# Kernel tuning notes

Measured on AMD Instinct MI355X. Metric: run time of the kernel, lower is better.

## Reference

```python
import jax, jax.numpy as jnp
import numpy as np

B, C_IN, H, W = 8, 64, 64, 64
C_OUT = 128
K, STRIDE, PAD = 3, 1, 1
GRID_MIN, GRID_MAX, NUM_GRIDS = -2.0, 2.0, 8
FEAT = C_IN * K * K  # 576


def setup_inputs() -> dict:
    key = jax.random.key(0)
    k1, k2, k3 = jax.random.split(key, 3)
    x = jax.random.normal(k1, (B, C_IN, H, W), dtype=jnp.float32)
    grid = jnp.linspace(GRID_MIN, GRID_MAX, NUM_GRIDS, dtype=jnp.float32)
    spline_weight = jax.random.normal(k2, (FEAT * NUM_GRIDS, C_OUT), dtype=jnp.float32) * 0.1
    # nn.Linear default init ~ U(-1/sqrt(in), 1/sqrt(in)); stored as (in, out) for x @ W
    bound = 1.0 / np.sqrt(FEAT)
    kw, kb = jax.random.split(k3)
    base_w = jax.random.uniform(kw, (FEAT, C_OUT), dtype=jnp.float32, minval=-bound, maxval=bound)
    base_b = jax.random.uniform(kb, (C_OUT,), dtype=jnp.float32, minval=-bound, maxval=bound)
    return {"x": x, "grid": grid, "spline_weight": spline_weight,
            "base_w": base_w, "base_b": base_b}


def reference(x, grid, spline_weight, base_w, base_b):
    b, c, h, w = x.shape
    # F.unfold equivalent: patches in (channel, kh, kw) channel-major order.
    patches = jax.lax.conv_general_dilated_patches(
        x, filter_shape=(K, K), window_strides=(STRIDE, STRIDE),
        padding=((PAD, PAD), (PAD, PAD)))  # [B, C*K*K, H', W']
    oh, ow = patches.shape[2], patches.shape[3]
    # -> [B*L, FEAT] rows, matching unfold().transpose(1,2).reshape(...)
    p = patches.reshape(b, FEAT, oh * ow).transpose(0, 2, 1).reshape(-1, FEAT)
    # RBF basis expansion: exp(-((x - g) / h)^2), h = grid spacing
    denom = (GRID_MAX - GRID_MIN) / (NUM_GRIDS - 1)
    basis = jnp.exp(-(((p[:, :, None] - grid) / denom) ** 2))  # [N, FEAT, G]
    ret = basis.reshape(p.shape[0], FEAT * NUM_GRIDS) @ spline_weight  # [N, C_OUT]
    ret = ret + jax.nn.silu(p) @ base_w + base_b
    # [B, L, C_OUT] -> [B, C_OUT, H', W']
    out = ret.reshape(b, oh * ow, C_OUT).transpose(0, 2, 1).reshape(b, C_OUT, oh, ow)
    return out
```

## Files before the change

kernel.cpp:

```cpp
#include <hip/hip_runtime.h>

#define C_IN   64
#define HW_DIM 64
#define C_OUT  128
#define NG     8
#define KSPL   4608
#define BM     64
#define NSPL_STEPS 72
#define NSTEPS 81
#define NPAD   66
#define NEXP   (8 * C_IN * NPAD * NPAD)

#define WT_BYTES 1327104
#define XE_OFF   WT_BYTES
#define XE_BYTES (NEXP * NG * 2)
#define SE_OFF   (XE_OFF + XE_BYTES)

typedef __attribute__((ext_vector_type(8))) __bf16 bf16x8;
typedef __attribute__((ext_vector_type(4))) float  f32x4;

__global__ __launch_bounds__(256)
void prep_wt(const float* __restrict__ sw, const float* __restrict__ bw,
             __bf16* __restrict__ wt3)
{
  const int step = blockIdx.x;
  const int t    = threadIdx.x;
  const int wc   = t >> 6;
  const int lane = t & 63;
  const int l15  = lane & 15;
  const int g4   = lane >> 4;
#pragma unroll
  for (int n = 0; n < 2; ++n)
#pragma unroll
    for (int ks = 0; ks < 2; ++ks) {
      const int co = wc * 32 + n * 16 + l15;
      bf16x8 v;
#pragma unroll
      for (int e = 0; e < 8; ++e) {
        const int k = step * 64 + ks * 32 + g4 * 8 + e;
        float f;
        if (k < KSPL) f = sw[(size_t)k * C_OUT + co];
        else          f = bw[(size_t)(k - KSPL) * C_OUT + co];
        v[e] = (__bf16)f;
      }
      *(bf16x8*)(wt3 + (size_t)step * 8192 + wc * 2048 + (n * 2 + ks) * 512
                 + lane * 8) = v;
    }
}

__global__ __launch_bounds__(256)
void expand(const float* __restrict__ x, const float* __restrict__ grid,
            __bf16* __restrict__ xe, __bf16* __restrict__ se)
{
  const int idx = blockIdx.x * 256 + threadIdx.x;
  if (idx >= NEXP) return;
  const int xp = idx % NPAD;
  const int r  = idx / NPAD;
  const int yp = r % NPAD;
  const int bc = r / NPAD;

  float p = 0.f;
  if (xp >= 1 && xp <= HW_DIM && yp >= 1 && yp <= HW_DIM)
    p = x[(size_t)bc * (HW_DIM * HW_DIM) + (yp - 1) * HW_DIM + (xp - 1)];

  bf16x8 v;
#pragma unroll
  for (int g = 0; g < NG; ++g) {
    const float z = 1.75f * (p - grid[g]);
    v[g] = (__bf16)__expf(-z * z);
  }
  *(bf16x8*)(xe + (size_t)idx * NG) = v;
  const float e = __expf(-p);
  se[idx] = (__bf16)(p * __builtin_amdgcn_rcpf(1.f + e));
}

static __device__ __forceinline__ void gload16(const __bf16* g, __bf16* l) {
  __builtin_amdgcn_global_load_lds(
      (const __attribute__((address_space(1))) void*)g,
      (__attribute__((address_space(3))) void*)l, 16, 0, 0);
}

#define WAITBAR6() do {                                      \
    asm volatile("s_waitcnt vmcnt(6)" ::: "memory");         \
    __builtin_amdgcn_s_barrier();                            \
    __builtin_amdgcn_sched_barrier(0);                       \
  } while (0)

__global__ __launch_bounds__(256, 2)
void kan_gemm(const __bf16* __restrict__ xe, const __bf16* __restrict__ se,
              const __bf16* __restrict__ wt3, const float* __restrict__ base_b,
              float* __restrict__ out)
{
  __shared__ __align__(16) __bf16 As[3][BM][64];
  __shared__ int tbl[576];

  const int t    = threadIdx.x;
  const int lane = t & 63;
  const int wid  = t >> 6;
  const int l15  = lane & 15;
  const int g4   = lane >> 4;

  const int bid = blockIdx.x;
  const int swz = (bid & 7) * 64 + (bid >> 3);
  const int b   = swz >> 6;
  const int y0  = swz & 63;

  for (int f = t; f < 576; f += 256) {
    const int c  = f / 9;
    const int j  = f - 9 * c;
    const int kh = j / 3;
    const int kw = j - 3 * kh;
    tbl[f] = c * 4356 + kh * 66 + kw;
  }

  const int ROW = b * 278784 + y0 * 66;

  const int qsrc  = (lane & 7) ^ ((lane >> 3) & 7);
  const int pbase = (wid << 3) + (lane >> 3);

  f32x4 acc[2][4];
#pragma unroll
  for (int n = 0; n < 2; ++n)
#pragma unroll
    for (int m = 0; m < 4; ++m)
      acc[n][m] = f32x4{0.f, 0.f, 0.f, 0.f};

  auto stageA = [&](int buf, int step) {
    const int off = ROW + tbl[step * 8 + qsrc] + pbase;
    __bf16* dst = &As[buf][0][0] + t * 8;
    gload16(xe + (size_t)off * 8,        dst);
    gload16(xe + (size_t)(off + 32) * 8, dst + 2048);
  };

  auto loadB = [&](bf16x8 (&wf)[2][2], int step) {
    const __bf16* wb = wt3 + (size_t)step * 8192 + wid * 2048 + lane * 8;
#pragma unroll
    for (int n = 0; n < 2; ++n)
#pragma unroll
      for (int ks = 0; ks < 2; ++ks)
        wf[n][ks] = *(const bf16x8*)(wb + (n * 2 + ks) * 512);
  };

  auto compute = [&](int buf, bf16x8 (&wf)[2][2]) {
    bf16x8 xf[4][2];
#pragma unroll
    for (int ks = 0; ks < 2; ++ks)
#pragma unroll
      for (int m = 0; m < 4; ++m) {
        const int pr = m * 16 + l15;
        xf[m][ks] = *(const bf16x8*)(&As[buf][pr][(((ks * 4 + g4) ^ (pr & 7)) * 8)]);
      }
#pragma unroll
    for (int ks = 0; ks < 2; ++ks)
#pragma unroll
      for (int n = 0; n < 2; ++n)
#pragma unroll
        for (int m = 0; m < 4; ++m)
          acc[n][m] = __builtin_amdgcn_mfma_f32_16x16x32_bf16(
              wf[n][ks], xf[m][ks], acc[n][m], 0, 0, 0);
  };

  __syncthreads();

  bf16x8 wA[2][2], wB[2][2], wC[2][2];
  stageA(0, 0); loadB(wA, 0);
  stageA(1, 1); loadB(wB, 1);
  WAITBAR6();

  for (int s = 0; s < 69; s += 3) {
    stageA(2, s + 2); loadB(wC, s + 2);
    compute(0, wA);
    WAITBAR6();
    stageA(0, s + 3); loadB(wA, s + 3);
    compute(1, wB);
    WAITBAR6();
    stageA(1, s + 4); loadB(wB, s + 4);
    compute(2, wC);
    WAITBAR6();
  }
  stageA(2, 71); loadB(wC, 71);
  compute(0, wA);
  WAITBAR6();
  compute(1, wB);
  asm volatile("s_waitcnt vmcnt(0)" ::: "memory");
  __builtin_amdgcn_s_barrier();
  __builtin_amdgcn_sched_barrier(0);
  compute(2, wC);

  const int ROWs = ROW + (t & 63);
  auto stageBase = [&](int buf, int bs) {
    const int px = t & 63;
#pragma unroll
    for (int h = 0; h < 2; ++h) {
      const int q = (t >> 6) + h * 4;
      bf16x8 v;
#pragma unroll
      for (int jj = 0; jj < 8; ++jj) {
        const int f = (bs - NSPL_STEPS) * 64 + q * 8 + jj;
        v[jj] = se[(size_t)(ROWs + tbl[f])];
      }
      *(bf16x8*)(&As[buf][px][(q ^ (px & 7)) * 8]) = v;
    }
  };

  stageBase(0, NSPL_STEPS);
  __syncthreads();
  for (int bs = NSPL_STEPS; bs < NSTEPS; ++bs) {
    const int cb = (bs - NSPL_STEPS) & 1;
    if (bs + 1 < NSTEPS) stageBase(cb ^ 1, bs + 1);
    loadB(wA, bs);
    compute(cb, wA);
    __syncthreads();
  }

#pragma unroll
  for (int n = 0; n < 2; ++n) {
    const int co = wid * 32 + n * 16 + g4 * 4;
#pragma unroll
    for (int m = 0; m < 4; ++m) {
      const int pl = m * 16 + l15;
      float* o = out + (size_t)(b * C_OUT + co) * 4096 + y0 * 64 + pl;
#pragma unroll
      for (int i = 0; i < 4; ++i)
        o[(size_t)i * 4096] = acc[n][m][i] + base_b[co + i];
    }
  }
}

extern "C" void kernel_launch(void* const* d_in, const int* in_sizes, int n_in,
                              void* d_out, int out_size, void* d_ws, size_t ws_size,
                              hipStream_t stream) {
  const float* x    = (const float*)d_in[0];
  const float* grid = (const float*)d_in[1];
  const float* sw   = (const float*)d_in[2];
  const float* bw   = (const float*)d_in[3];
  const float* bb   = (const float*)d_in[4];
  float* out = (float*)d_out;

  __bf16* wt3 = (__bf16*)d_ws;
  __bf16* xe  = (__bf16*)((char*)d_ws + XE_OFF);
  __bf16* se  = (__bf16*)((char*)d_ws + SE_OFF);

  prep_wt<<<NSTEPS, 256, 0, stream>>>(sw, bw, wt3);
  expand<<<(NEXP + 255) / 256, 256, 0, stream>>>(x, grid, xe, se);
  kan_gemm<<<512, 256, 0, stream>>>(xe, se, wt3, bb, out);
}
```

Before: 78.85 us.

## Double GEMM block tile to two output rows with 512 threads

Each block now covers two output rows (128 pixels) with 8 waves instead of one row with 4 waves. Each pair of waves shares the same weight columns, and the grid halves to 256 blocks. The goal is more reuse of the staged tiles and fewer blocks re-reading weights. In exchange the shared tile doubles in size, and with only 256 blocks occupancy or load balance across CUs may suffer.

```diff
diff --git a/kernel.cpp b/kernel.cpp
--- a/kernel.cpp
+++ b/kernel.cpp
@@ -5,7 +5,7 @@
 #define C_OUT  128
 #define NG     8
 #define KSPL   4608
-#define BM     64
+#define BM     128
 #define NSPL_STEPS 72
 #define NSTEPS 81
 #define NPAD   66
@@ -25,7 +25,7 @@
 {
   const int step = blockIdx.x;
   const int t    = threadIdx.x;
-  const int wc   = t >> 6;
+  const int nq   = t >> 6;
   const int lane = t & 63;
   const int l15  = lane & 15;
   const int g4   = lane >> 4;
@@ -33,7 +33,7 @@
   for (int n = 0; n < 2; ++n)
 #pragma unroll
     for (int ks = 0; ks < 2; ++ks) {
-      const int co = wc * 32 + n * 16 + l15;
+      const int co = nq * 32 + n * 16 + l15;
       bf16x8 v;
 #pragma unroll
       for (int e = 0; e < 8; ++e) {
@@ -43,7 +43,7 @@
         else          f = bw[(size_t)(k - KSPL) * C_OUT + co];
         v[e] = (__bf16)f;
       }
-      *(bf16x8*)(wt3 + (size_t)step * 8192 + wc * 2048 + (n * 2 + ks) * 512
+      *(bf16x8*)(wt3 + (size_t)step * 8192 + nq * 2048 + (n * 2 + ks) * 512
                  + lane * 8) = v;
     }
 }
@@ -86,7 +86,7 @@
     __builtin_amdgcn_sched_barrier(0);                       \
   } while (0)
 
-__global__ __launch_bounds__(256, 2)
+__global__ __launch_bounds__(512, 2)
 void kan_gemm(const __bf16* __restrict__ xe, const __bf16* __restrict__ se,
               const __bf16* __restrict__ wt3, const float* __restrict__ base_b,
               float* __restrict__ out)
@@ -99,13 +99,15 @@
   const int wid  = t >> 6;
   const int l15  = lane & 15;
   const int g4   = lane >> 4;
+  const int mh   = wid >> 2;
+  const int nq   = wid & 3;
 
   const int bid = blockIdx.x;
-  const int swz = (bid & 7) * 64 + (bid >> 3);
-  const int b   = swz >> 6;
-  const int y0  = swz & 63;
-
-  for (int f = t; f < 576; f += 256) {
+  const int swz = (bid & 7) * 32 + (bid >> 3);
+  const int b   = swz >> 5;
+  const int y0  = (swz & 31) * 2;
+
+  for (int f = t; f < 576; f += 512) {
     const int c  = f / 9;
     const int j  = f - 9 * c;
     const int kh = j / 3;
@@ -115,8 +117,8 @@
 
   const int ROW = b * 278784 + y0 * 66;
 
-  const int qsrc  = (lane & 7) ^ ((lane >> 3) & 7);
-  const int pbase = (wid << 3) + (lane >> 3);
+  const int qsrc = (t & 7) ^ ((t >> 3) & 7);
+  const int xcol = t >> 3;
 
   f32x4 acc[2][4];
 #pragma unroll
@@ -126,14 +128,14 @@
       acc[n][m] = f32x4{0.f, 0.f, 0.f, 0.f};
 
   auto stageA = [&](int buf, int step) {
-    const int off = ROW + tbl[step * 8 + qsrc] + pbase;
+    const int off = ROW + tbl[step * 8 + qsrc] + xcol;
     __bf16* dst = &As[buf][0][0] + t * 8;
     gload16(xe + (size_t)off * 8,        dst);
-    gload16(xe + (size_t)(off + 32) * 8, dst + 2048);
+    gload16(xe + (size_t)(off + 66) * 8, dst + 4096);
   };
 
   auto loadB = [&](bf16x8 (&wf)[2][2], int step) {
-    const __bf16* wb = wt3 + (size_t)step * 8192 + wid * 2048 + lane * 8;
+    const __bf16* wb = wt3 + (size_t)step * 8192 + nq * 2048 + lane * 8;
 #pragma unroll
     for (int n = 0; n < 2; ++n)
 #pragma unroll
@@ -147,7 +149,7 @@
     for (int ks = 0; ks < 2; ++ks)
 #pragma unroll
       for (int m = 0; m < 4; ++m) {
-        const int pr = m * 16 + l15;
+        const int pr = mh * 64 + m * 16 + l15;
         xf[m][ks] = *(const bf16x8*)(&As[buf][pr][(((ks * 4 + g4) ^ (pr & 7)) * 8)]);
       }
 #pragma unroll
@@ -187,19 +189,18 @@
   __builtin_amdgcn_sched_barrier(0);
   compute(2, wC);
 
-  const int ROWs = ROW + (t & 63);
   auto stageBase = [&](int buf, int bs) {
-    const int px = t & 63;
 #pragma unroll
     for (int h = 0; h < 2; ++h) {
-      const int q = (t >> 6) + h * 4;
+      const int px    = h * 64 + (t >> 3);
+      const int gslot = t & 7;
       bf16x8 v;
 #pragma unroll
       for (int jj = 0; jj < 8; ++jj) {
-        const int f = (bs - NSPL_STEPS) * 64 + q * 8 + jj;
-        v[jj] = se[(size_t)(ROWs + tbl[f])];
+        const int f = (bs - NSPL_STEPS) * 64 + qsrc * 8 + jj;
+        v[jj] = se[(size_t)(ROW + tbl[f] + (px >> 6) * 66 + (px & 63))];
       }
-      *(bf16x8*)(&As[buf][px][(q ^ (px & 7)) * 8]) = v;
+      *(bf16x8*)(&As[buf][px][gslot * 8]) = v;
     }
   };
 
@@ -215,11 +216,12 @@
 
 #pragma unroll
   for (int n = 0; n < 2; ++n) {
-    const int co = wid * 32 + n * 16 + g4 * 4;
+    const int co = nq * 32 + n * 16 + g4 * 4;
 #pragma unroll
     for (int m = 0; m < 4; ++m) {
-      const int pl = m * 16 + l15;
-      float* o = out + (size_t)(b * C_OUT + co) * 4096 + y0 * 64 + pl;
+      const int y = y0 + mh;
+      const int xcoord = m * 16 + l15;
+      float* o = out + (size_t)(b * C_OUT + co) * 4096 + y * 64 + xcoord;
 #pragma unroll
       for (int i = 0; i < 4; ++i)
         o[(size_t)i * 4096] = acc[n][m][i] + base_b[co + i];
@@ -243,5 +245,5 @@
 
   prep_wt<<<NSTEPS, 256, 0, stream>>>(sw, bw, wt3);
   expand<<<(NEXP + 255) / 256, 256, 0, stream>>>(x, grid, xe, se);
-  kan_gemm<<<512, 256, 0, stream>>>(xe, se, wt3, bb, out);
-}
+  kan_gemm<<<256, 512, 0, stream>>>(xe, se, wt3, bb, out);
+}
```

Result: slower. 97.55 us (+23.7%).

## Double spline K-step width to 128 and split base weights into separate layout

Applied to the files above, without the earlier changes.

The spline GEMM main loop now processes 128 K-elements per pipeline stage (36 stages instead of 72). The weight prep is reorganised into a 128-wide spline layout plus a separate 64-wide base section, and a new XOR swizzle is applied to the wider LDS tile. MFMA sections are wrapped in s_setprio to favour matrix issue. The goal is to halve the barrier and wait count per unit of work and give more work between syncs. The cost is double the LDS footprint and more weight registers, which may reduce occupancy at two blocks per CU.

```diff
diff --git a/kernel.cpp b/kernel.cpp
--- a/kernel.cpp
+++ b/kernel.cpp
@@ -6,16 +6,19 @@
 #define NG     8
 #define KSPL   4608
 #define BM     64
-#define NSPL_STEPS 72
-#define NSTEPS 81
+#define NIV    36
+#define NBASE  9
 #define NPAD   66
 #define NEXP   (8 * C_IN * NPAD * NPAD)
 
+#define BOFF     589824
 #define WT_BYTES 1327104
 #define XE_OFF   WT_BYTES
 #define XE_BYTES (NEXP * NG * 2)
 #define SE_OFF   (XE_OFF + XE_BYTES)
 
+#define SW(c, p) (((c) & 8) | (((c) ^ (p)) & 7))
+
 typedef __attribute__((ext_vector_type(8))) __bf16 bf16x8;
 typedef __attribute__((ext_vector_type(4))) float  f32x4;
 
@@ -23,29 +26,45 @@
 void prep_wt(const float* __restrict__ sw, const float* __restrict__ bw,
              __bf16* __restrict__ wt3)
 {
-  const int step = blockIdx.x;
+  const int bid  = blockIdx.x;
   const int t    = threadIdx.x;
-  const int wc   = t >> 6;
+  const int cq   = t >> 6;
   const int lane = t & 63;
   const int l15  = lane & 15;
   const int g4   = lane >> 4;
-#pragma unroll
-  for (int n = 0; n < 2; ++n)
-#pragma unroll
-    for (int ks = 0; ks < 2; ++ks) {
-      const int co = wc * 32 + n * 16 + l15;
-      bf16x8 v;
-#pragma unroll
-      for (int e = 0; e < 8; ++e) {
-        const int k = step * 64 + ks * 32 + g4 * 8 + e;
-        float f;
-        if (k < KSPL) f = sw[(size_t)k * C_OUT + co];
-        else          f = bw[(size_t)(k - KSPL) * C_OUT + co];
-        v[e] = (__bf16)f;
-      }
-      *(bf16x8*)(wt3 + (size_t)step * 8192 + wc * 2048 + (n * 2 + ks) * 512
-                 + lane * 8) = v;
-    }
+  if (bid < NIV) {
+    const int iv = bid;
+#pragma unroll
+    for (int n = 0; n < 2; ++n)
+#pragma unroll
+      for (int ks = 0; ks < 4; ++ks) {
+        const int co = cq * 32 + n * 16 + l15;
+        bf16x8 v;
+#pragma unroll
+        for (int e = 0; e < 8; ++e) {
+          const int k = iv * 128 + ks * 32 + g4 * 8 + e;
+          v[e] = (__bf16)sw[(size_t)k * C_OUT + co];
+        }
+        *(bf16x8*)(wt3 + (size_t)iv * 16384 + cq * 4096 + (n * 4 + ks) * 512
+                   + lane * 8) = v;
+      }
+  } else {
+    const int bs = bid - NIV;
+#pragma unroll
+    for (int n = 0; n < 2; ++n)
+#pragma unroll
+      for (int ks = 0; ks < 2; ++ks) {
+        const int co = cq * 32 + n * 16 + l15;
+        bf16x8 v;
+#pragma unroll
+        for (int e = 0; e < 8; ++e) {
+          const int kb = bs * 64 + ks * 32 + g4 * 8 + e;
+          v[e] = (__bf16)bw[(size_t)kb * C_OUT + co];
+        }
+        *(bf16x8*)(wt3 + (size_t)BOFF + bs * 8192 + cq * 2048 + (n * 2 + ks) * 512
+                   + lane * 8) = v;
+      }
+  }
 }
 
 __global__ __launch_bounds__(256)
@@ -80,8 +99,8 @@
       (__attribute__((address_space(3))) void*)l, 16, 0, 0);
 }
 
-#define WAITBAR6() do {                                      \
-    asm volatile("s_waitcnt vmcnt(6)" ::: "memory");         \
+#define WAITBAR12() do {                                     \
+    asm volatile("s_waitcnt vmcnt(12)" ::: "memory");        \
     __builtin_amdgcn_s_barrier();                            \
     __builtin_amdgcn_sched_barrier(0);                       \
   } while (0)
@@ -91,7 +110,7 @@
               const __bf16* __restrict__ wt3, const float* __restrict__ base_b,
               float* __restrict__ out)
 {
-  __shared__ __align__(16) __bf16 As[3][BM][64];
+  __shared__ __align__(16) __bf16 AsF[3 * 64 * 128];
   __shared__ int tbl[576];
 
   const int t    = threadIdx.x;
@@ -115,9 +134,6 @@
 
   const int ROW = b * 278784 + y0 * 66;
 
-  const int qsrc  = (lane & 7) ^ ((lane >> 3) & 7);
-  const int pbase = (wid << 3) + (lane >> 3);
-
   f32x4 acc[2][4];
 #pragma unroll
   for (int n = 0; n < 2; ++n)
@@ -125,91 +141,128 @@
     for (int m = 0; m < 4; ++m)
       acc[n][m] = f32x4{0.f, 0.f, 0.f, 0.f};
 
-  auto stageA = [&](int buf, int step) {
-    const int off = ROW + tbl[step * 8 + qsrc] + pbase;
-    __bf16* dst = &As[buf][0][0] + t * 8;
-    gload16(xe + (size_t)off * 8,        dst);
-    gload16(xe + (size_t)(off + 32) * 8, dst + 2048);
-  };
-
-  auto loadB = [&](bf16x8 (&wf)[2][2], int step) {
-    const __bf16* wb = wt3 + (size_t)step * 8192 + wid * 2048 + lane * 8;
+  auto stageA = [&](int buf, int iv) {
+    const int gslot = t & 15;
+    __bf16* dst = AsF + buf * 8192 + t * 8;
+#pragma unroll
+    for (int p = 0; p < 4; ++p) {
+      const int px  = p * 16 + (t >> 4);
+      const int f   = iv * 16 + SW(gslot, px);
+      const int off = ROW + tbl[f] + px;
+      gload16(xe + (size_t)off * 8, dst + p * 2048);
+    }
+  };
+
+  auto loadB = [&](bf16x8 (&wf)[2][4], int iv) {
+    const __bf16* wb = wt3 + (size_t)iv * 16384 + wid * 4096 + lane * 8;
 #pragma unroll
     for (int n = 0; n < 2; ++n)
 #pragma unroll
-      for (int ks = 0; ks < 2; ++ks)
-        wf[n][ks] = *(const bf16x8*)(wb + (n * 2 + ks) * 512);
-  };
-
-  auto compute = [&](int buf, bf16x8 (&wf)[2][2]) {
-    bf16x8 xf[4][2];
-#pragma unroll
-    for (int ks = 0; ks < 2; ++ks)
+      for (int ks = 0; ks < 4; ++ks)
+        wf[n][ks] = *(const bf16x8*)(wb + (n * 4 + ks) * 512);
+  };
+
+  auto compute = [&](int buf, bf16x8 (&wf)[2][4]) {
+    __builtin_amdgcn_s_setprio(1);
+#pragma unroll
+    for (int ks = 0; ks < 4; ++ks) {
+      const int gidx = ks * 4 + g4;
+      bf16x8 xf[4];
 #pragma unroll
       for (int m = 0; m < 4; ++m) {
         const int pr = m * 16 + l15;
-        xf[m][ks] = *(const bf16x8*)(&As[buf][pr][(((ks * 4 + g4) ^ (pr & 7)) * 8)]);
-      }
-#pragma unroll
-    for (int ks = 0; ks < 2; ++ks)
+        xf[m] = *(const bf16x8*)(AsF + buf * 8192 + pr * 128 + SW(gidx, pr) * 8);
+      }
 #pragma unroll
       for (int n = 0; n < 2; ++n)
 #pragma unroll
         for (int m = 0; m < 4; ++m)
           acc[n][m] = __builtin_amdgcn_mfma_f32_16x16x32_bf16(
-              wf[n][ks], xf[m][ks], acc[n][m], 0, 0, 0);
+              wf[n][ks], xf[m], acc[n][m], 0, 0, 0);
+    }
+    __builtin_amdgcn_s_setprio(0);
   };
 
   __syncthreads();
 
-  bf16x8 wA[2][2], wB[2][2], wC[2][2];
+  bf16x8 wA[2][4], wB[2][4], wC[2][4];
   stageA(0, 0); loadB(wA, 0);
   stageA(1, 1); loadB(wB, 1);
-  WAITBAR6();
-
-  for (int s = 0; s < 69; s += 3) {
+  WAITBAR12();
+
+  for (int s = 0; s < 33; s += 3) {
     stageA(2, s + 2); loadB(wC, s + 2);
     compute(0, wA);
-    WAITBAR6();
+    WAITBAR12();
     stageA(0, s + 3); loadB(wA, s + 3);
     compute(1, wB);
-    WAITBAR6();
+    WAITBAR12();
     stageA(1, s + 4); loadB(wB, s + 4);
     compute(2, wC);
-    WAITBAR6();
-  }
-  stageA(2, 71); loadB(wC, 71);
+    WAITBAR12();
+  }
+  stageA(2, 35); loadB(wC, 35);
   compute(0, wA);
-  WAITBAR6();
+  WAITBAR12();
   compute(1, wB);
   asm volatile("s_waitcnt vmcnt(0)" ::: "memory");
   __builtin_amdgcn_s_barrier();
   __builtin_amdgcn_sched_barrier(0);
   compute(2, wC);
 
-  const int ROWs = ROW + (t & 63);
   auto stageBase = [&](int buf, int bs) {
     const int px = t & 63;
 #pragma unroll
     for (int h = 0; h < 2; ++h) {
-      const int q = (t >> 6) + h * 4;
+      const int gslot = (t >> 6) + h * 4;
+      const int q     = gslot ^ (px & 7);
       bf16x8 v;
 #pragma unroll
       for (int jj = 0; jj < 8; ++jj) {
-        const int f = (bs - NSPL_STEPS) * 64 + q * 8 + jj;
-        v[jj] = se[(size_t)(ROWs + tbl[f])];
-      }
-      *(bf16x8*)(&As[buf][px][(q ^ (px & 7)) * 8]) = v;
-    }
-  };
-
-  stageBase(0, NSPL_STEPS);
+        const int f = bs * 64 + q * 8 + jj;
+        v[jj] = se[(size_t)(ROW + tbl[f] + px)];
+      }
+      *(bf16x8*)(AsF + buf * 8192 + px * 64 + gslot * 8) = v;
+    }
+  };
+
+  auto loadBbase = [&](bf16x8 (&wf)[2][2], int bs) {
+    const __bf16* wb = wt3 + (size_t)BOFF + bs * 8192 + wid * 2048 + lane * 8;
+#pragma unroll
+    for (int n = 0; n < 2; ++n)
+#pragma unroll
+      for (int ks = 0; ks < 2; ++ks)
+        wf[n][ks] = *(const bf16x8*)(wb + (n * 2 + ks) * 512);
+  };
+
+  auto computeBase = [&](int buf, bf16x8 (&wf)[2][2]) {
+#pragma unroll
+    for (int ks = 0; ks < 2; ++ks) {
+      const int gidx = ks * 4 + g4;
+      bf16x8 xf[4];
+#pragma unroll
+      for (int m = 0; m < 4; ++m) {
+        const int pr = m * 16 + l15;
+        xf[m] = *(const bf16x8*)(AsF + buf * 8192 + pr * 64
+                                 + (gidx ^ (pr & 7)) * 8);
+      }
+#pragma unroll
+      for (int n = 0; n < 2; ++n)
+#pragma unroll
+        for (int m = 0; m < 4; ++m)
+          acc[n][m] = __builtin_amdgcn_mfma_f32_16x16x32_bf16(
+              wf[n][ks], xf[m], acc[n][m], 0, 0, 0);
+    }
+  };
+
+  stageBase(0, 0);
   __syncthreads();
-  for (int bs = NSPL_STEPS; bs < NSTEPS; ++bs) {
-    const int cb = (bs - NSPL_STEPS) & 1;
-    if (bs + 1 < NSTEPS) stageBase(cb ^ 1, bs + 1);
-    loadB(wA, bs);
-    compute(cb, wA);
+  bf16x8 wD[2][2];
+  for (int bs = 0; bs < NBASE; ++bs) {
+    const int cb = bs & 1;
+    if (bs + 1 < NBASE) stageBase(cb ^ 1, bs + 1);
+    loadBbase(wD, bs);
+    computeBase(cb, wD);
     __syncthreads();
   }
 
@@ -241,7 +294,7 @@
   __bf16* xe  = (__bf16*)((char*)d_ws + XE_OFF);
   __bf16* se  = (__bf16*)((char*)d_ws + SE_OFF);
 
-  prep_wt<<<NSTEPS, 256, 0, stream>>>(sw, bw, wt3);
+  prep_wt<<<NIV + NBASE, 256, 0, stream>>>(sw, bw, wt3);
   expand<<<(NEXP + 255) / 256, 256, 0, stream>>>(x, grid, xe, se);
   kan_gemm<<<512, 256, 0, stream>>>(xe, se, wt3, bb, out);
 }
```

Result: slower. 87.98 us (+11.6%).

## Split spline K dimension across two blocks with atomic accumulation

Applied to the files above, without the earlier changes.

Each output tile is now computed by two blocks that each handle half of the spline reduction steps. One of the two also runs the base SiLU steps. A separate kernel pre-fills the output with the bias, and partial sums are combined with float atomic adds. Occupancy hint is raised to 4 blocks per CU. The aim is to fill more CUs and shorten the per-block serial K loop, at the cost of an extra launch, atomic read-modify-write traffic on the output, and uneven work between the two halves.

```diff
diff --git a/kernel.cpp b/kernel.cpp
--- a/kernel.cpp
+++ b/kernel.cpp
@@ -8,6 +8,8 @@
 #define BM     64
 #define NSPL_STEPS 72
 #define NSTEPS 81
+#define NHALF  36
+#define NBASE  9
 #define NPAD   66
 #define NEXP   (8 * C_IN * NPAD * NPAD)
 
@@ -74,6 +76,15 @@
   se[idx] = (__bf16)(p * __builtin_amdgcn_rcpf(1.f + e));
 }
 
+__global__ __launch_bounds__(256)
+void init_out(const float* __restrict__ bb, float* __restrict__ out)
+{
+  const int i4 = blockIdx.x * 256 + threadIdx.x;
+  const int e  = i4 * 4;
+  const float v = bb[(e >> 12) & 127];
+  *(f32x4*)(out + e) = f32x4{v, v, v, v};
+}
+
 static __device__ __forceinline__ void gload16(const __bf16* g, __bf16* l) {
   __builtin_amdgcn_global_load_lds(
       (const __attribute__((address_space(1))) void*)g,
@@ -86,10 +97,9 @@
     __builtin_amdgcn_sched_barrier(0);                       \
   } while (0)
 
-__global__ __launch_bounds__(256, 2)
+__global__ __launch_bounds__(256, 4)
 void kan_gemm(const __bf16* __restrict__ xe, const __bf16* __restrict__ se,
-              const __bf16* __restrict__ wt3, const float* __restrict__ base_b,
-              float* __restrict__ out)
+              const __bf16* __restrict__ wt3, float* __restrict__ out)
 {
   __shared__ __align__(16) __bf16 As[3][BM][64];
   __shared__ int tbl[576];
@@ -101,16 +111,19 @@
   const int g4   = lane >> 4;
 
   const int bid = blockIdx.x;
-  const int swz = (bid & 7) * 64 + (bid >> 3);
-  const int b   = swz >> 6;
-  const int y0  = swz & 63;
+  const int swz = (bid & 7) * 128 + (bid >> 3);
+  const int kh  = swz & 1;
+  const int rb  = swz >> 1;
+  const int b   = rb >> 6;
+  const int y0  = rb & 63;
+  const int S0  = kh * NHALF;
 
   for (int f = t; f < 576; f += 256) {
     const int c  = f / 9;
     const int j  = f - 9 * c;
-    const int kh = j / 3;
-    const int kw = j - 3 * kh;
-    tbl[f] = c * 4356 + kh * 66 + kw;
+    const int kk = j / 3;
+    const int kw = j - 3 * kk;
+    tbl[f] = c * 4356 + kk * 66 + kw;
   }
 
   const int ROW = b * 278784 + y0 * 66;
@@ -163,22 +176,22 @@
   __syncthreads();
 
   bf16x8 wA[2][2], wB[2][2], wC[2][2];
-  stageA(0, 0); loadB(wA, 0);
-  stageA(1, 1); loadB(wB, 1);
+  stageA(0, S0 + 0); loadB(wA, S0 + 0);
+  stageA(1, S0 + 1); loadB(wB, S0 + 1);
   WAITBAR6();
 
-  for (int s = 0; s < 69; s += 3) {
-    stageA(2, s + 2); loadB(wC, s + 2);
+  for (int s = 0; s < NHALF - 3; s += 3) {
+    stageA(2, S0 + s + 2); loadB(wC, S0 + s + 2);
     compute(0, wA);
     WAITBAR6();
-    stageA(0, s + 3); loadB(wA, s + 3);
+    stageA(0, S0 + s + 3); loadB(wA, S0 + s + 3);
     compute(1, wB);
     WAITBAR6();
-    stageA(1, s + 4); loadB(wB, s + 4);
+    stageA(1, S0 + s + 4); loadB(wB, S0 + s + 4);
     compute(2, wC);
     WAITBAR6();
   }
-  stageA(2, 71); loadB(wC, 71);
+  stageA(2, S0 + 35); loadB(wC, S0 + 35);
   compute(0, wA);
   WAITBAR6();
   compute(1, wB);
@@ -187,30 +200,35 @@
   __builtin_amdgcn_sched_barrier(0);
   compute(2, wC);
 
-  const int ROWs = ROW + (t & 63);
-  auto stageBase = [&](int buf, int bs) {
-    const int px = t & 63;
-#pragma unroll
-    for (int h = 0; h < 2; ++h) {
-      const int q = (t >> 6) + h * 4;
-      bf16x8 v;
-#pragma unroll
-      for (int jj = 0; jj < 8; ++jj) {
-        const int f = (bs - NSPL_STEPS) * 64 + q * 8 + jj;
-        v[jj] = se[(size_t)(ROWs + tbl[f])];
+  if (kh == 1) {
+    const int ROWs = ROW + (t & 63);
+    auto stageBase = [&](int buf, int bs) {
+      const int px = t & 63;
+#pragma unroll
+      for (int h = 0; h < 2; ++h) {
+        const int q = (t >> 6) + h * 4;
+        bf16x8 v;
+#pragma unroll
+        for (int jj = 0; jj < 8; ++jj) {
+          const int f = bs * 64 + q * 8 + jj;
+          v[jj] = se[(size_t)(ROWs + tbl[f])];
+        }
+        *(bf16x8*)(&As[buf][px][((q ^ (px & 7)) * 8)]) = v;
       }
-      *(bf16x8*)(&As[buf][px][(q ^ (px & 7)) * 8]) = v;
+    };
+    auto loadBbase = [&](bf16x8 (&wf)[2][2], int bs) {
+      loadB(wf, NSPL_STEPS + bs);
+    };
+
+    stageBase(0, 0);
+    __syncthreads();
+    for (int bs = 0; bs < NBASE; ++bs) {
+      const int cb = bs & 1;
+      if (bs + 1 < NBASE) stageBase(cb ^ 1, bs + 1);
+      loadBbase(wA, bs);
+      compute(cb, wA);
+      __syncthreads();
     }
-  };
-
-  stageBase(0, NSPL_STEPS);
-  __syncthreads();
-  for (int bs = NSPL_STEPS; bs < NSTEPS; ++bs) {
-    const int cb = (bs - NSPL_STEPS) & 1;
-    if (bs + 1 < NSTEPS) stageBase(cb ^ 1, bs + 1);
-    loadB(wA, bs);
-    compute(cb, wA);
-    __syncthreads();
   }
 
 #pragma unroll
@@ -222,7 +240,7 @@
       float* o = out + (size_t)(b * C_OUT + co) * 4096 + y0 * 64 + pl;
 #pragma unroll
       for (int i = 0; i < 4; ++i)
-        o[(size_t)i * 4096] = acc[n][m][i] + base_b[co + i];
+        unsafeAtomicAdd(o + (size_t)i * 4096, acc[n][m][i]);
     }
   }
 }
@@ -243,5 +261,6 @@
 
   prep_wt<<<NSTEPS, 256, 0, stream>>>(sw, bw, wt3);
   expand<<<(NEXP + 255) / 256, 256, 0, stream>>>(x, grid, xe, se);
-  kan_gemm<<<512, 256, 0, stream>>>(xe, se, wt3, bb, out);
-}
+  init_out<<<4096, 256, 0, stream>>>(bb, out);
+  kan_gemm<<<1024, 256, 0, stream>>>(xe, se, wt3, out);
+}
```

New measurement: 91.95 us. 1.17x slower.
